# Kernel optimization log

Measured on AMD Instinct MI355X. Metric: run time of the kernel, lower is better.

## Reference

```python
import jax, jax.numpy as jnp
import numpy as np

KSIZE = 3
SOFTMAX_SCALE = 10.0


def extract_patches(x):
    # x: [B, C, H, W] -> patches [B, H*W, C, 3, 3]
    # Matches F.unfold(same_padding(x), kernel=3, stride=1) then
    # reshape(B, C, 3, 3, L).permute(0, 4, 1, 2, 3).
    B, C, H, W = x.shape
    xp = jnp.pad(x, ((0, 0), (0, 0), (1, 1), (1, 1)))
    # p[b, c, i, j, y, x] = xp[b, c, y+i, x+j]
    p = jnp.stack(
        [jnp.stack([xp[:, :, i:i + H, j:j + W] for j in range(KSIZE)], axis=2)
         for i in range(KSIZE)], axis=2)  # [B, C, 3, 3, H, W]
    return p.transpose(0, 4, 5, 1, 2, 3).reshape(B, H * W, C, KSIZE, KSIZE)


def _conv_same(x, w):
    # x: [Cin, H, W], w: [Cout, Cin, 3, 3] -> [Cout, H, W] (pad 1, stride 1)
    return jax.lax.conv_general_dilated(
        x[None], w, window_strides=(1, 1), padding=((1, 1), (1, 1)),
        dimension_numbers=('NCHW', 'OIHW', 'NCHW'))[0]


def setup_inputs() -> dict:
    key = jax.random.key(0)
    kf, kb = jax.random.split(key)
    f = jax.random.normal(kf, (4, 64, 64, 64), dtype=jnp.float32)
    b = jax.random.normal(kb, (4, 64, 64, 64), dtype=jnp.float32)
    return {"f": f, "b": b}


def reference(f, b):
    B, C, Hf, Wf = f.shape
    # Per-sample dynamic kernels from background patches: [B, L, C, 3, 3]
    w = extract_patches(b)
    # Correlation: per-sample conv of f with its own L patch-kernels -> [B, L, Hf, Wf]
    scores = jax.vmap(_conv_same)(f, w)
    # Scaled softmax over the L patch axis
    attn = jax.nn.softmax(scores * SOFTMAX_SCALE, axis=1)
    # conv_transpose2d(attn, w, stride=1, padding=1) == SAME conv with
    # spatially-flipped kernels and in/out channels swapped.
    w_t = jnp.flip(w, axis=(-2, -1)).transpose(0, 2, 1, 3, 4)  # [B, C, L, 3, 3]
    y = jax.vmap(_conv_same)(attn, w_t) / 9.0  # [B, C, Hf, Wf]
    return (y, w.reshape(B, -1, KSIZE, KSIZE))
```

## Files before the change

### kernel.cpp

```cpp
#include <hip/hip_runtime.h>
#include <hip/hip_bf16.h>
#include <hip/hip_fp16.h>
#include <stdint.h>


typedef unsigned short ushort_t;
typedef __attribute__((ext_vector_type(8))) short bf16x8;
typedef __attribute__((ext_vector_type(4))) float f32x4;

__device__ __forceinline__ float bf2f(ushort_t u){
  union { float f; uint32_t i; } v; v.i = ((uint32_t)u) << 16; return v.f;
}
__device__ __forceinline__ ushort_t f2bf(float f){
  union { float f; uint32_t i; } v; v.f = f;
  uint32_t x = v.i;
  return (ushort_t)((x + 0x7fffu + ((x >> 16) & 1u)) >> 16);
}

__global__ __launch_bounds__(256) void k_prep(const float* __restrict__ bin,
                                              float* __restrict__ wout,
                                              float* __restrict__ yzero){
  int t = blockIdx.x * 256 + threadIdx.x;
  yzero[t] = 0.f;
  int c  = t & 63;
  int l  = (t >> 6) & 4095;
  int bb = t >> 18;
  int y = l >> 6, x = l & 63;
  const float* src = bin + (((size_t)(bb * 64 + c)) << 12);
  float* dst = wout + (size_t)t * 9;
  #pragma unroll
  for (int i = 0; i < 3; i++){
    int yy = y + i - 1;
    #pragma unroll
    for (int j = 0; j < 3; j++){
      int xx = x + j - 1;
      float v = 0.f;
      if ((unsigned)yy < 64u && (unsigned)xx < 64u) v = src[(yy << 6) + xx];
      dst[i * 3 + j] = v;
    }
  }
}

__global__ __launch_bounds__(256, 2) void k_rgemm(const float* __restrict__ f,
                                                  const float* __restrict__ bin,
                                                  float* __restrict__ R,
                                                  int bt0){
  __shared__ float As[64][128];
  __shared__ float Bs[64][128];
  int bt = bt0 + blockIdx.z;
  int m0 = blockIdx.x << 7;
  int n0 = blockIdx.y << 7;
  const float* fb = f   + (((size_t)bt) << 18);
  const float* bb = bin + (((size_t)bt) << 18);
  int t = threadIdx.x;
  for (int idx = t; idx < 64 * 128; idx += 256){
    int c = idx >> 7, m = idx & 127;
    As[c][m] = fb[(c << 12) + m0 + m];
    Bs[c][m] = bb[(c << 12) + n0 + m];
  }
  __syncthreads();
  int tx = t & 15, ty = t >> 4;
  float acc[8][8];
  #pragma unroll
  for (int i = 0; i < 8; i++)
    #pragma unroll
    for (int j = 0; j < 8; j++) acc[i][j] = 0.f;

  for (int c = 0; c < 64; c++){
    float4 a0 = *(const float4*)&As[c][(ty << 3)];
    float4 a1 = *(const float4*)&As[c][(ty << 3) + 4];
    float4 b0 = *(const float4*)&Bs[c][(tx << 2)];
    float4 b1 = *(const float4*)&Bs[c][64 + (tx << 2)];
    float av[8] = {a0.x, a0.y, a0.z, a0.w, a1.x, a1.y, a1.z, a1.w};
    float bv[8] = {b0.x, b0.y, b0.z, b0.w, b1.x, b1.y, b1.z, b1.w};
    #pragma unroll
    for (int i = 0; i < 8; i++)
      #pragma unroll
      for (int j = 0; j < 8; j++) acc[i][j] += av[i] * bv[j];
  }
  #pragma unroll
  for (int i = 0; i < 8; i++){
    float* dst = R + ((size_t)(m0 + (ty << 3) + i) << 12) + n0;
    *(float4*)(dst + (tx << 2))      = make_float4(acc[i][0], acc[i][1], acc[i][2], acc[i][3]);
    *(float4*)(dst + 64 + (tx << 2)) = make_float4(acc[i][4], acc[i][5], acc[i][6], acc[i][7]);
  }
}

__global__ __launch_bounds__(256, 2) void k_softmax4(const float* __restrict__ R,
                                                     ushort_t* __restrict__ attn,
                                                     float* __restrict__ scale){
  __shared__ float Rt[24][648];
  const int t  = threadIdx.x;
  const int bb = blockIdx.x;
  const int inner = bb >> 3;
  const int ty = ((bb & 7) << 1) | (inner & 1);
  const int tx = inner >> 1;
  const int p0 = ty << 2, q0 = tx << 1;
  const int qi = t >> 5, kt = t & 31;
  const int pi = qi >> 1, qj = qi & 1;
  const int ktx = kt & 15;

  float M = -3.0e38f, L = 0.f;
  float mref[8];
  float4 rbuf[16];

  int row = ((p0 + pi) << 6) + q0 + qj;
  ushort_t* arow = attn + ((size_t)row << 12);

  #pragma unroll
  for (int i = 0; i < 16; i++){
    int idx = t + (i << 8);
    float4 v = make_float4(0.f, 0.f, 0.f, 0.f);
    if (idx < 3888){
      unsigned r = (unsigned)idx / 162u;
      int fo = idx - (int)r * 162;
      int rp = p0 - 1 + (int)(r >> 2);
      int rq = q0 - 1 + (int)(r & 3);
      int kg = -68 + (fo << 2);
      if ((unsigned)rp < 64u && (unsigned)rq < 64u && (unsigned)kg <= 4092u)
        v = *(const float4*)(R + (((size_t)((rp << 6) + rq)) << 12) + kg);
    }
    rbuf[i] = v;
  }

  #pragma unroll
  for (int c = 0; c < 8; c++){
    __syncthreads();
    #pragma unroll
    for (int i = 0; i < 16; i++){
      int idx = t + (i << 8);
      if (idx < 3888) ((float4*)&Rt[0][0])[idx] = rbuf[i];
    }
    __syncthreads();
    if (c < 7){
      const int k0 = (c + 1) << 9;
      #pragma unroll
      for (int i = 0; i < 16; i++){
        int idx = t + (i << 8);
        float4 v = make_float4(0.f, 0.f, 0.f, 0.f);
        if (idx < 3888){
          unsigned r = (unsigned)idx / 162u;
          int fo = idx - (int)r * 162;
          int rp = p0 - 1 + (int)(r >> 2);
          int rq = q0 - 1 + (int)(r & 3);
          int kg = k0 - 68 + (fo << 2);
          if ((unsigned)rp < 64u && (unsigned)rq < 64u && (unsigned)kg <= 4092u)
            v = *(const float4*)(R + (((size_t)((rp << 6) + rq)) << 12) + kg);
        }
        rbuf[i] = v;
      }
    }
    float4 sv[4];
    #pragma unroll
    for (int j = 0; j < 4; j++){
      int y = (c << 3) + (j << 1) + (kt >> 4);
      int sa0 = (j << 7) + (kt << 2) + 68;
      float4 s = make_float4(0.f, 0.f, 0.f, 0.f);
      #pragma unroll
      for (int a = -1; a <= 1; a++){
        if ((unsigned)(y + a) < 64u){
          int rb = (pi + 1 + a) << 2;
          int sa = sa0 + (a << 6);
          float4 A0 = *(const float4*)&Rt[rb + qj][sa];
          float4 A1 = *(const float4*)&Rt[rb + qj + 1][sa];
          float4 A2 = *(const float4*)&Rt[rb + qj + 2][sa];
          float Lv = __shfl_up(A0.w, 1);
          float Rv = __shfl_down(A2.x, 1);
          s.x += (ktx == 0 ? 0.f : Lv) + A1.x + A2.y;
          s.y += A0.x + A1.y + A2.z;
          s.z += A0.y + A1.z + A2.w;
          s.w += A0.z + A1.w + (ktx == 15 ? 0.f : Rv);
        }
      }
      s.x *= 10.f; s.y *= 10.f; s.z *= 10.f; s.w *= 10.f;
      sv[j] = s;
    }
    float mc = M;
    #pragma unroll
    for (int j = 0; j < 4; j++)
      mc = fmaxf(mc, fmaxf(fmaxf(sv[j].x, sv[j].y), fmaxf(sv[j].z, sv[j].w)));
    #pragma unroll
    for (int off = 1; off < 32; off <<= 1) mc = fmaxf(mc, __shfl_xor(mc, off));
    float lnew = L * __expf(M - mc);
    #pragma unroll
    for (int j = 0; j < 4; j++){
      float ex = __expf(sv[j].x - mc), ey = __expf(sv[j].y - mc);
      float ez = __expf(sv[j].z - mc), ew = __expf(sv[j].w - mc);
      lnew += ex + ey + ez + ew;
      ushort4 o; o.x = f2bf(ex); o.y = f2bf(ey); o.z = f2bf(ez); o.w = f2bf(ew);
      *(ushort4*)&arow[(c << 9) + (j << 7) + (kt << 2)] = o;
    }
    L = lnew; M = mc; mref[c] = mc;
  }
  #pragma unroll
  for (int off = 1; off < 32; off <<= 1) L += __shfl_xor(L, off);
  if (kt == 0){
    float invL = 1.0f / L;
    float4 s0, s1;
    s0.x = __expf(mref[0] - M) * invL; s0.y = __expf(mref[1] - M) * invL;
    s0.z = __expf(mref[2] - M) * invL; s0.w = __expf(mref[3] - M) * invL;
    s1.x = __expf(mref[4] - M) * invL; s1.y = __expf(mref[5] - M) * invL;
    s1.z = __expf(mref[6] - M) * invL; s1.w = __expf(mref[7] - M) * invL;
    *(float4*)&scale[(row << 3)]     = s0;
    *(float4*)&scale[(row << 3) + 4] = s1;
  }
}

__global__ __launch_bounds__(256, 2) void k_pstencil5(const ushort_t* __restrict__ attn,
                                                      const float* __restrict__ scale,
                                                      ushort_t* __restrict__ P){
  __shared__ float At[24][648];
  __shared__ float Sc[24][8];
  const int t  = threadIdx.x;
  const int bb = blockIdx.x;
  const int inner = bb >> 3;
  const int ty = ((bb & 7) << 1) | (inner & 1);
  const int tx = inner >> 1;
  const int p0 = ty << 2, q0 = tx << 1;
  const int qi = t >> 5, kt = t & 31;
  const int pi = qi >> 1, qj = qi & 1;
  const int ktx = kt & 15;

  int row = ((p0 + pi) << 6) + q0 + qj;
  ushort_t* prow = P + ((size_t)row << 12);
  const float inv9 = 1.0f / 9.0f;

  if (t < 192){
    int r = t >> 3, cc = t & 7;
    int rp = p0 - 1 + (r >> 2);
    int rq = q0 - 1 + (r & 3);
    float v = 0.f;
    if ((unsigned)rp < 64u && (unsigned)rq < 64u)
      v = scale[(((rp << 6) + rq) << 3) + cc];
    Sc[r][cc] = v;
  }

  uint2 rbuf[16];
  #pragma unroll
  for (int i = 0; i < 16; i++){
    int idx = t + (i << 8);
    uint2 v = make_uint2(0u, 0u);
    if (idx < 3888){
      unsigned r = (unsigned)idx / 162u;
      int fo = idx - (int)r * 162;
      int rp = p0 - 1 + (int)(r >> 2);
      int rq = q0 - 1 + (int)(r & 3);
      int kg = -68 + (fo << 2);
      if ((unsigned)rp < 64u && (unsigned)rq < 64u && (unsigned)kg <= 4092u)
        v = *(const uint2*)(attn + (((size_t)((rp << 6) + rq)) << 12) + kg);
    }
    rbuf[i] = v;
  }

  #pragma unroll
  for (int c = 0; c < 8; c++){
    __syncthreads();
    #pragma unroll
    for (int i = 0; i < 16; i++){
      int idx = t + (i << 8);
      if (idx < 3888){
        unsigned r = (unsigned)idx / 162u;
        int fo = idx - (int)r * 162;
        int key = (c << 9) - 68 + (fo << 2);
        key = key < 0 ? 0 : (key > 4095 ? 4095 : key);
        float sc = Sc[r][key >> 9];
        uint2 u = rbuf[i];
        float4 w;
        { union { uint32_t q; float f; } a_, b_;
          a_.q = u.x << 16; b_.q = u.x & 0xffff0000u; w.x = a_.f * sc; w.y = b_.f * sc; }
        { union { uint32_t q; float f; } a_, b_;
          a_.q = u.y << 16; b_.q = u.y & 0xffff0000u; w.z = a_.f * sc; w.w = b_.f * sc; }
        ((float4*)&At[0][0])[idx] = w;
      }
    }
    __syncthreads();
    if (c < 7){
      const int k0 = (c + 1) << 9;
      #pragma unroll
      for (int i = 0; i < 16; i++){
        int idx = t + (i << 8);
        uint2 v = make_uint2(0u, 0u);
        if (idx < 3888){
          unsigned r = (unsigned)idx / 162u;
          int fo = idx - (int)r * 162;
          int rp = p0 - 1 + (int)(r >> 2);
          int rq = q0 - 1 + (int)(r & 3);
          int kg = k0 - 68 + (fo << 2);
          if ((unsigned)rp < 64u && (unsigned)rq < 64u && (unsigned)kg <= 4092u)
            v = *(const uint2*)(attn + (((size_t)((rp << 6) + rq)) << 12) + kg);
        }
        rbuf[i] = v;
      }
    }
    #pragma unroll
    for (int j = 0; j < 4; j++){
      int y = (c << 3) + (j << 1) + (kt >> 4);
      int sa0 = (j << 7) + (kt << 2) + 68;
      float4 s = make_float4(0.f, 0.f, 0.f, 0.f);
      #pragma unroll
      for (int a = -1; a <= 1; a++){
        if ((unsigned)(y + a) < 64u){
          int rb = (pi + 1 + a) << 2;
          int sa = sa0 + (a << 6);
          float4 A0 = *(const float4*)&At[rb + qj][sa];
          float4 A1 = *(const float4*)&At[rb + qj + 1][sa];
          float4 A2 = *(const float4*)&At[rb + qj + 2][sa];
          float Lv = __shfl_up(A0.w, 1);
          float Rv = __shfl_down(A2.x, 1);
          s.x += (ktx == 0 ? 0.f : Lv) + A1.x + A2.y;
          s.y += A0.x + A1.y + A2.z;
          s.z += A0.y + A1.z + A2.w;
          s.w += A0.z + A1.w + (ktx == 15 ? 0.f : Rv);
        }
      }
      ushort4 o;
      o.x = f2bf(s.x * inv9);
      o.y = f2bf(s.y * inv9);
      o.z = f2bf(s.z * inv9);
      o.w = f2bf(s.w * inv9);
      *(ushort4*)&prow[(c << 9) + (j << 7) + (kt << 2)] = o;
    }
  }
}

__global__ __launch_bounds__(256) void k_ygemm(const float* __restrict__ bin,
                                               const ushort_t* __restrict__ P,
                                               float* __restrict__ y,
                                               int bt0){
  __shared__ ushort_t SB[64][72];
  __shared__ ushort_t SP[64][72];
  int bt  = bt0 + blockIdx.z;
  int pq0 = blockIdx.x << 6;
  int k0  = blockIdx.y << 10;
  int t = threadIdx.x;
  int lane = t & 63, wv = t >> 6;
  const float*    bbase = bin + (((size_t)bt) << 18);
  const ushort_t* Pbase = P + ((size_t)pq0 << 12);

  f32x4 acc[4];
  #pragma unroll
  for (int cb = 0; cb < 4; cb++) acc[cb] = (f32x4){0.f, 0.f, 0.f, 0.f};

  for (int kb = k0; kb < k0 + 1024; kb += 64){
    for (int idx = t; idx < 1024; idx += 256){
      int c = idx >> 4, g = idx & 15;
      float4 v = *(const float4*)(bbase + (c << 12) + kb + (g << 2));
      ushort_t* d = &SB[c][g << 2];
      d[0] = f2bf(v.x); d[1] = f2bf(v.y); d[2] = f2bf(v.z); d[3] = f2bf(v.w);
    }
    for (int idx = t; idx < 1024; idx += 256){
      int r = idx >> 4, g = idx & 15;
      *(uint64_t*)&SP[r][g << 2] =
          *(const uint64_t*)(Pbase + (((size_t)r) << 12) + kb + (g << 2));
    }
    __syncthreads();
    #pragma unroll
    for (int ks = 0; ks < 64; ks += 32){
      bf16x8 pf = *(const bf16x8*)&SP[(wv << 4) + (lane & 15)][ks + ((lane >> 4) << 3)];
      #pragma unroll
      for (int cb = 0; cb < 4; cb++){
        bf16x8 bf = *(const bf16x8*)&SB[(cb << 4) + (lane & 15)][ks + ((lane >> 4) << 3)];
        acc[cb] = __builtin_amdgcn_mfma_f32_16x16x32_bf16(bf, pf, acc[cb], 0, 0, 0);
      }
    }
    __syncthreads();
  }
  int quad = lane >> 4;
  int pql = pq0 + (wv << 4) + (lane & 15);
  #pragma unroll
  for (int cb = 0; cb < 4; cb++)
    #pragma unroll
    for (int r = 0; r < 4; r++){
      int c = (cb << 4) + (quad << 2) + r;
      atomicAdd(&y[(((size_t)(bt * 64 + c)) << 12) + pql], acc[cb][r]);
    }
}

extern "C" void kernel_launch(void* const* d_in, const int* in_sizes, int n_in,
                              void* d_out, int out_size, void* d_ws, size_t ws_size,
                              hipStream_t stream){
  const float* f = (const float*)d_in[0];
  const float* b = (const float*)d_in[1];
  float* out  = (float*)d_out;
  float* yout = out;
  float* wout = out + 1048576;

  const size_t RB  = 4096ull * 4096 * 4;
  const size_t AB  = 4096ull * 4096 * 2;
  const size_t SCB = 4096ull * 8 * 4;
  (void)SCB;

  k_prep<<<4096, 256, 0, stream>>>(b, wout, yout);

  float*    R     = (float*)d_ws;
  ushort_t* attn  = (ushort_t*)((char*)d_ws + RB);
  float*    scale = (float*)((char*)d_ws + RB + AB);
  ushort_t* P     = (ushort_t*)d_ws;
  for (int bt = 0; bt < 4; bt++){
    k_rgemm    <<<dim3(32, 32, 1), 256, 0, stream>>>(f, b, R, bt);
    k_softmax4 <<<512, 256, 0, stream>>>(R, attn, scale);
    k_pstencil5<<<512, 256, 0, stream>>>(attn, scale, P);
    k_ygemm    <<<dim3(64, 4, 1), 256, 0, stream>>>(b, P, yout, bt);
  }
}
```

Measured before the change: 701.6 us.

## Rewrite y-GEMM to load MFMA operands directly from global and split K finer

The y-GEMM kernel no longer stages B and P tiles through shared memory with barriers. Each lane now loads its MFMA fragments straight from global memory, converting B to bf16 in registers. The K range per block shrinks from 1024 to 256, so the grid grows from 4 to 16 blocks along K. This removes LDS traffic and synchronisation and adds parallelism, but it repeats global loads and bf16 conversions of B across waves and quadruples the atomicAdd traffic into y.

```diff
diff --git a/kernel.cpp b/kernel.cpp
--- a/kernel.cpp
+++ b/kernel.cpp
@@ -323,50 +323,40 @@
   }
 }
 
-__global__ __launch_bounds__(256) void k_ygemm(const float* __restrict__ bin,
-                                               const ushort_t* __restrict__ P,
-                                               float* __restrict__ y,
-                                               int bt0){
-  __shared__ ushort_t SB[64][72];
-  __shared__ ushort_t SP[64][72];
-  int bt  = bt0 + blockIdx.z;
-  int pq0 = blockIdx.x << 6;
-  int k0  = blockIdx.y << 10;
-  int t = threadIdx.x;
-  int lane = t & 63, wv = t >> 6;
+__global__ __launch_bounds__(256) void k_ygemm2(const float* __restrict__ bin,
+                                                const ushort_t* __restrict__ P,
+                                                float* __restrict__ y,
+                                                int bt){
+  const int t = threadIdx.x;
+  const int lane = t & 63, wv = t >> 6;
+  const int n = lane & 15, quad = lane >> 4;
+  const int pq0 = blockIdx.x << 6;
+  const int k0  = blockIdx.y << 8;
   const float*    bbase = bin + (((size_t)bt) << 18);
-  const ushort_t* Pbase = P + ((size_t)pq0 << 12);
+  const ushort_t* Prow  = P + (((size_t)(pq0 + (wv << 4) + n)) << 12);
 
   f32x4 acc[4];
   #pragma unroll
   for (int cb = 0; cb < 4; cb++) acc[cb] = (f32x4){0.f, 0.f, 0.f, 0.f};
 
-  for (int kb = k0; kb < k0 + 1024; kb += 64){
-    for (int idx = t; idx < 1024; idx += 256){
-      int c = idx >> 4, g = idx & 15;
-      float4 v = *(const float4*)(bbase + (c << 12) + kb + (g << 2));
-      ushort_t* d = &SB[c][g << 2];
-      d[0] = f2bf(v.x); d[1] = f2bf(v.y); d[2] = f2bf(v.z); d[3] = f2bf(v.w);
-    }
-    for (int idx = t; idx < 1024; idx += 256){
-      int r = idx >> 4, g = idx & 15;
-      *(uint64_t*)&SP[r][g << 2] =
-          *(const uint64_t*)(Pbase + (((size_t)r) << 12) + kb + (g << 2));
-    }
-    __syncthreads();
-    #pragma unroll
-    for (int ks = 0; ks < 64; ks += 32){
-      bf16x8 pf = *(const bf16x8*)&SP[(wv << 4) + (lane & 15)][ks + ((lane >> 4) << 3)];
-      #pragma unroll
-      for (int cb = 0; cb < 4; cb++){
-        bf16x8 bf = *(const bf16x8*)&SB[(cb << 4) + (lane & 15)][ks + ((lane >> 4) << 3)];
-        acc[cb] = __builtin_amdgcn_mfma_f32_16x16x32_bf16(bf, pf, acc[cb], 0, 0, 0);
-      }
-    }
-    __syncthreads();
-  }
-  int quad = lane >> 4;
-  int pql = pq0 + (wv << 4) + (lane & 15);
+  #pragma unroll 2
+  for (int kb = k0; kb < k0 + 256; kb += 32){
+    int ko = kb + (quad << 3);
+    bf16x8 pf = *(const bf16x8*)(Prow + ko);
+    #pragma unroll
+    for (int cb = 0; cb < 4; cb++){
+      const float* bp = bbase + (((cb << 4) + n) << 12) + ko;
+      float4 b0 = *(const float4*)bp;
+      float4 b1 = *(const float4*)(bp + 4);
+      bf16x8 bf;
+      bf[0] = (short)f2bf(b0.x); bf[1] = (short)f2bf(b0.y);
+      bf[2] = (short)f2bf(b0.z); bf[3] = (short)f2bf(b0.w);
+      bf[4] = (short)f2bf(b1.x); bf[5] = (short)f2bf(b1.y);
+      bf[6] = (short)f2bf(b1.z); bf[7] = (short)f2bf(b1.w);
+      acc[cb] = __builtin_amdgcn_mfma_f32_16x16x32_bf16(bf, pf, acc[cb], 0, 0, 0);
+    }
+  }
+  int pql = pq0 + (wv << 4) + n;
   #pragma unroll
   for (int cb = 0; cb < 4; cb++)
     #pragma unroll
@@ -387,8 +377,6 @@
 
   const size_t RB  = 4096ull * 4096 * 4;
   const size_t AB  = 4096ull * 4096 * 2;
-  const size_t SCB = 4096ull * 8 * 4;
-  (void)SCB;
 
   k_prep<<<4096, 256, 0, stream>>>(b, wout, yout);
 
@@ -400,6 +388,6 @@
     k_rgemm    <<<dim3(32, 32, 1), 256, 0, stream>>>(f, b, R, bt);
     k_softmax4 <<<512, 256, 0, stream>>>(R, attn, scale);
     k_pstencil5<<<512, 256, 0, stream>>>(attn, scale, P);
-    k_ygemm    <<<dim3(64, 4, 1), 256, 0, stream>>>(b, P, yout, bt);
-  }
-}
+    k_ygemm2   <<<dim3(64, 16), 256, 0, stream>>>(b, P, yout, bt);
+  }
+}
```

Measured after the change: 663.0 us. 5.5% less time.
